# Performance work log

Measured on AMD Instinct MI355X. Metric: run time of the kernel, lower is better.

Reference implementation:

```python
import jax, jax.numpy as jnp
import numpy as np

IN_FEATURES = 8192
OUT_FEATURES = 8192
BITS = 4
TILE = 16
M_TOKENS = 64  # small token count -> dequant-traffic dominated (memory regime)
SCALE_BLOCK = 128


def setup_inputs() -> dict:
    key = jax.random.key(0)
    k1, k2, k3, k4, k5, k6 = jax.random.split(key, 6)
    tiles_k = IN_FEATURES // TILE
    tiles_n = OUT_FEATURES // TILE
    packed_bytes = 256 * BITS // 8  # 128 bytes per 16x16 tile for 4-bit
    x = jax.random.normal(k1, (M_TOKENS, IN_FEATURES), dtype=jnp.float32)
    packed_indices = jax.random.randint(k2, (tiles_k, tiles_n, packed_bytes), 0, 256, dtype=jnp.int32)
    scales = jax.random.uniform(k3, ((IN_FEATURES + SCALE_BLOCK - 1) // SCALE_BLOCK, OUT_FEATURES), dtype=jnp.float32, minval=0.5, maxval=1.5)
    su = jax.random.normal(k4, (IN_FEATURES,), dtype=jnp.float32)
    sv = jax.random.normal(k5, (OUT_FEATURES,), dtype=jnp.float32)
    grid = jax.random.normal(k6, (2 ** BITS,), dtype=jnp.float32)  # trellis codebook grid
    return {"x": x, "packed_indices": packed_indices, "scales": scales, "su": su, "sv": sv, "grid": grid}


def _dequantize(packed_indices, scales, su, sv, grid):
    # packed_indices: [tiles_k, tiles_n, packed_bytes] byte values (0..255)
    tk, tn, pb = packed_indices.shape
    bits = (pb * 8) // (TILE * TILE)
    # unpack bytes -> bits (little-endian within byte), then group into bits-per-index
    bitplane = (packed_indices[..., None] >> jnp.arange(8, dtype=jnp.int32)) & 1  # [tk, tn, pb, 8]
    idx = (bitplane.reshape(tk, tn, TILE * TILE, bits)
           * (2 ** jnp.arange(bits, dtype=jnp.int32))).sum(-1)  # [tk, tn, 256]
    vals = grid[idx].reshape(tk, tn, TILE, TILE)  # tile element order: (k_in_tile, n_in_tile)
    # assemble full weight laid out [K_in, N_out]
    W = vals.transpose(0, 2, 1, 3).reshape(tk * TILE, tn * TILE)
    # per-128-row-block scales over the K dim
    nb = scales.shape[0]
    W = (W.reshape(nb, SCALE_BLOCK, tn * TILE) * scales[:, None, :]).reshape(tk * TILE, tn * TILE)
    # per-row (su) and per-column (sv) scale/sign vectors
    W = W * su[:, None] * sv[None, :]
    return W  # [in_features, out_features]


def reference(x, packed_indices, scales, su, sv, grid):
    W = _dequantize(packed_indices, scales, su, sv, grid)  # [K, N]
    # torch: x.view(-1, K) @ weights[N, K].T  ==  x @ W[K, N]
    lead = x.shape[:-1]
    out = x.reshape(-1, W.shape[0]) @ W
    return out.reshape(*lead, W.shape[1])
```

## Files before the change

kernel.cpp:

```cpp
#include <hip/hip_runtime.h>

typedef float f32x4 __attribute__((ext_vector_type(4)));
typedef __bf16 bf16x8 __attribute__((ext_vector_type(8)));

#define K_FEAT 8192
#define N_FEAT 8192
#define M_TOK 64
#define TILES_N 512
#define TILES_K 512
#define WROWSTRIDE 40
#define LG_KSPLIT 3
#define KSPLIT 8
#define NSTEP 32

__device__ __forceinline__ unsigned short f2bf(float f) {
    unsigned int u = __builtin_bit_cast(unsigned int, f);
    u = (u + 0x7FFFu + ((u >> 16) & 1u)) >> 16;
    return (unsigned short)u;
}
__device__ __forceinline__ float bf2f(unsigned short h) {
    return __builtin_bit_cast(float, (unsigned int)h << 16);
}

__global__ void __launch_bounds__(256)
prep_x_kernel(const float* __restrict__ x, const float* __restrict__ su,
              unsigned short* __restrict__ xb)
{
    int i = blockIdx.x * 256 + threadIdx.x;
    const float4* x4 = (const float4*)x;
    const float4* su4 = (const float4*)su;
    float4 xv = x4[i];
    float4 s4 = su4[i & (K_FEAT / 4 - 1)];
    ushort4 o;
    o.x = f2bf(xv.x * s4.x);
    o.y = f2bf(xv.y * s4.y);
    o.z = f2bf(xv.z * s4.z);
    o.w = f2bf(xv.w * s4.w);
    ((ushort4*)xb)[i] = o;
}

__global__ void __launch_bounds__(256)
trellis_main(const int* __restrict__ packed,
             const float* __restrict__ scales,
             const float* __restrict__ sv,
             const float* __restrict__ grid,
             const unsigned short* __restrict__ xb,
             unsigned short* __restrict__ partials)
{
    __shared__ unsigned int table[256];
    __shared__ unsigned short wlds[2][64 * WROWSTRIDE];
    __shared__ float slds[8 * 64];

    const int tid = threadIdx.x;
    const int bid = blockIdx.x;
    const int s = bid & (KSPLIT - 1);
    const int ng = bid >> LG_KSPLIT;
    const int col0 = ng * 64;
    const int nt0 = ng * 4;
    const int ktile0 = s * (TILES_K / KSPLIT);

    const int tau = tid >> 5;
    const int dkt = tau >> 2;
    const int dnt_s = tau & 3;
    const int w = tid & 31;
    const int c = w & 7;
    const int g = w >> 3;

    const int* pb = packed
        + ((size_t)(ktile0 + dkt) * TILES_N + (nt0 + dnt_s)) * 128 + c + 32 * g;
    const int stepstride = 2 * TILES_N * 128;

    const int wave = tid >> 6;
    const int lane = tid & 63;
    const int ln15 = lane & 15;
    const int kgrp = (lane >> 4) * 8;
    const unsigned short* xrow = xb + (size_t)(wave * 16 + ln15) * K_FEAT;

    {
        float lo = grid[tid & 15];
        float hi = grid[(tid >> 4) & 15];
        table[tid] = (unsigned int)f2bf(lo) | ((unsigned int)f2bf(hi) << 16);
    }
    {
        const int kb0 = s * 8;
        slds[tid]       = scales[(size_t)(kb0 + (tid >> 6)) * N_FEAT + col0 + (tid & 63)];
        slds[tid + 256] = scales[(size_t)(kb0 + 4 + (tid >> 6)) * N_FEAT + col0 + (tid & 63)];
    }

    int ld0 = pb[0], ld1 = pb[8], ld2 = pb[16], ld3 = pb[24];
    uint4 ra = *(const uint4*)(xrow + ktile0 * 16 + kgrp);

    f32x4 acc[4], acc2[4];
    for (int d = 0; d < 4; ++d)
        for (int j = 0; j < 4; ++j) { acc[d][j] = 0.f; acc2[d][j] = 0.f; }

    __syncthreads();

    for (int t = 0; t < NSTEP; ++t) {
        int n0 = 0, n1 = 0, n2 = 0, n3 = 0;
        if (t + 1 < NSTEP) {
            const int* pn = pb + (size_t)(t + 1) * stepstride;
            n0 = pn[0]; n1 = pn[8]; n2 = pn[16]; n3 = pn[24];
        }

        unsigned int t0 = table[ld0 & 255];
        unsigned int t1 = table[ld1 & 255];
        unsigned int t2 = table[ld2 & 255];
        unsigned int t3 = table[ld3 & 255];
        unsigned int w0 = (t0 & 0xFFFFu) | (t1 << 16);
        unsigned int w1 = (t2 & 0xFFFFu) | (t3 << 16);
        unsigned int w2 = (t0 >> 16)     | (t1 & 0xFFFF0000u);
        unsigned int w3 = (t2 >> 16)     | (t3 & 0xFFFF0000u);
        {
            int nrow = dnt_s * 16 + 2 * c;
            int koff = dkt * 16 + 4 * g;
            unsigned short* dst = &wlds[t & 1][nrow * WROWSTRIDE + koff];
            *(uint2*)dst = make_uint2(w0, w1);
            *(uint2*)(dst + WROWSTRIDE) = make_uint2(w2, w3);
        }

        __builtin_amdgcn_sched_barrier(0);
        asm volatile("s_waitcnt lgkmcnt(0)" ::: "memory");
        __builtin_amdgcn_s_barrier();
        __builtin_amdgcn_sched_barrier(0);

        int k0n = ktile0 * 16 + (t + 1 < NSTEP ? (t + 1) : 0) * 32;
        uint4 ran = *(const uint4*)(xrow + k0n + kgrp);

        bf16x8 a = __builtin_bit_cast(bf16x8, ra);
        const unsigned short* wbase = &wlds[t & 1][0];
        for (int d = 0; d < 4; ++d) {
            bf16x8 b = *(const bf16x8*)(wbase + (d * 16 + ln15) * WROWSTRIDE + kgrp);
            acc2[d] = __builtin_amdgcn_mfma_f32_16x16x32_bf16(a, b, acc2[d], 0, 0, 0);
        }
        ra = ran;
        ld0 = n0; ld1 = n1; ld2 = n2; ld3 = n3;

        if ((t & 3) == 3) {
            const float* srow = slds + (t >> 2) * 64 + ln15;
            for (int d = 0; d < 4; ++d) {
                float sc = srow[d * 16];
                acc[d] += acc2[d] * sc;
                for (int j = 0; j < 4; ++j) acc2[d][j] = 0.f;
            }
        }
    }

    unsigned short* pout = partials + (size_t)s * (M_TOK * N_FEAT);
    const int rbase = (lane >> 4) * 4;
    for (int d = 0; d < 4; ++d) {
        int n = col0 + d * 16 + ln15;
        float svv = sv[n];
        for (int j = 0; j < 4; ++j) {
            int m = wave * 16 + rbase + j;
            pout[(size_t)m * N_FEAT + n] = f2bf(acc[d][j] * svv);
        }
    }
}

__global__ void __launch_bounds__(256)
reduce_kernel(const unsigned short* __restrict__ partials, float* __restrict__ out)
{
    int i = blockIdx.x * 256 + threadIdx.x;
    const uint4* p = (const uint4*)partials;
    float acc[8];
    for (int e = 0; e < 8; ++e) acc[e] = 0.f;
    for (int k = 0; k < KSPLIT; ++k) {
        uint4 v = p[(size_t)k * (M_TOK * N_FEAT / 8) + i];
        unsigned int uu[4] = {v.x, v.y, v.z, v.w};
        for (int q = 0; q < 4; ++q) {
            acc[2 * q]     += bf2f((unsigned short)(uu[q] & 0xFFFFu));
            acc[2 * q + 1] += bf2f((unsigned short)(uu[q] >> 16));
        }
    }
    float4 o0 = make_float4(acc[0], acc[1], acc[2], acc[3]);
    float4 o1 = make_float4(acc[4], acc[5], acc[6], acc[7]);
    ((float4*)out)[2 * i]     = o0;
    ((float4*)out)[2 * i + 1] = o1;
}

extern "C" void kernel_launch(void* const* d_in, const int* in_sizes, int n_in,
                              void* d_out, int out_size, void* d_ws, size_t ws_size,
                              hipStream_t stream)
{
    const float* x      = (const float*)d_in[0];
    const int*   packed = (const int*)d_in[1];
    const float* scales = (const float*)d_in[2];
    const float* su     = (const float*)d_in[3];
    const float* sv     = (const float*)d_in[4];
    const float* grid   = (const float*)d_in[5];
    float* out = (float*)d_out;

    unsigned short* xb = (unsigned short*)d_ws;
    const size_t xb_bytes = (size_t)M_TOK * K_FEAT * 2;
    unsigned short* partials = (unsigned short*)((char*)d_ws + xb_bytes);

    prep_x_kernel<<<(M_TOK * K_FEAT / 4) / 256, 256, 0, stream>>>(x, su, xb);
    trellis_main<<<(N_FEAT / 64) * KSPLIT, 256, 0, stream>>>(
        packed, scales, sv, grid, xb, partials);
    reduce_kernel<<<(M_TOK * N_FEAT / 8) / 256, 256, 0, stream>>>(partials, out);
}
```

Baseline: 38.04 us.

## Fuse split-K reduction into main kernel via last-block atomic counter; deepen packed prefetch

Removes the separate reduce kernel. Each block increments a per-column-group counter, and the last of the KSPLIT blocks sums the bf16 partials and writes the fp32 output. This saves a launch and its tail, at the cost of an added memset, fences and a serialized reduction tail inside the last block. The packed-index prefetch is also deepened to two steps ahead so more load latency is hidden, at the cost of more registers.

```diff
diff --git a/kernel.cpp b/kernel.cpp
--- a/kernel.cpp
+++ b/kernel.cpp
@@ -12,6 +12,7 @@
 #define LG_KSPLIT 3
 #define KSPLIT 8
 #define NSTEP 32
+#define NGROUPS (N_FEAT / 64)
 
 __device__ __forceinline__ unsigned short f2bf(float f) {
     unsigned int u = __builtin_bit_cast(unsigned int, f);
@@ -45,11 +46,14 @@
              const float* __restrict__ sv,
              const float* __restrict__ grid,
              const unsigned short* __restrict__ xb,
-             unsigned short* __restrict__ partials)
+             unsigned short* __restrict__ partials,
+             int* __restrict__ counters,
+             float* __restrict__ out)
 {
     __shared__ unsigned int table[256];
     __shared__ unsigned short wlds[2][64 * WROWSTRIDE];
     __shared__ float slds[8 * 64];
+    __shared__ int is_last;
 
     const int tid = threadIdx.x;
     const int bid = blockIdx.x;
@@ -87,7 +91,9 @@
         slds[tid + 256] = scales[(size_t)(kb0 + 4 + (tid >> 6)) * N_FEAT + col0 + (tid & 63)];
     }
 
-    int ld0 = pb[0], ld1 = pb[8], ld2 = pb[16], ld3 = pb[24];
+    int a0 = pb[0], a1 = pb[8], a2 = pb[16], a3 = pb[24];
+    const int* p1 = pb + stepstride;
+    int b0 = p1[0], b1 = p1[8], b2 = p1[16], b3 = p1[24];
     uint4 ra = *(const uint4*)(xrow + ktile0 * 16 + kgrp);
 
     f32x4 acc[4], acc2[4];
@@ -97,16 +103,14 @@
     __syncthreads();
 
     for (int t = 0; t < NSTEP; ++t) {
-        int n0 = 0, n1 = 0, n2 = 0, n3 = 0;
-        if (t + 1 < NSTEP) {
-            const int* pn = pb + (size_t)(t + 1) * stepstride;
-            n0 = pn[0]; n1 = pn[8]; n2 = pn[16]; n3 = pn[24];
-        }
-
-        unsigned int t0 = table[ld0 & 255];
-        unsigned int t1 = table[ld1 & 255];
-        unsigned int t2 = table[ld2 & 255];
-        unsigned int t3 = table[ld3 & 255];
+        const int tc = (t + 2 < NSTEP) ? (t + 2) : (NSTEP - 1);
+        const int* pn = pb + (size_t)tc * stepstride;
+        int c0 = pn[0], c1 = pn[8], c2 = pn[16], c3 = pn[24];
+
+        unsigned int t0 = table[a0 & 255];
+        unsigned int t1 = table[a1 & 255];
+        unsigned int t2 = table[a2 & 255];
+        unsigned int t3 = table[a3 & 255];
         unsigned int w0 = (t0 & 0xFFFFu) | (t1 << 16);
         unsigned int w1 = (t2 & 0xFFFFu) | (t3 << 16);
         unsigned int w2 = (t0 >> 16)     | (t1 & 0xFFFF0000u);
@@ -134,7 +138,8 @@
             acc2[d] = __builtin_amdgcn_mfma_f32_16x16x32_bf16(a, b, acc2[d], 0, 0, 0);
         }
         ra = ran;
-        ld0 = n0; ld1 = n1; ld2 = n2; ld3 = n3;
+        a0 = b0; a1 = b1; a2 = b2; a3 = b3;
+        b0 = c0; b1 = c1; b2 = c2; b3 = c3;
 
         if ((t & 3) == 3) {
             const float* srow = slds + (t >> 2) * 64 + ln15;
@@ -156,27 +161,34 @@
             pout[(size_t)m * N_FEAT + n] = f2bf(acc[d][j] * svv);
         }
     }
-}
-
-__global__ void __launch_bounds__(256)
-reduce_kernel(const unsigned short* __restrict__ partials, float* __restrict__ out)
-{
-    int i = blockIdx.x * 256 + threadIdx.x;
-    const uint4* p = (const uint4*)partials;
-    float acc[8];
-    for (int e = 0; e < 8; ++e) acc[e] = 0.f;
-    for (int k = 0; k < KSPLIT; ++k) {
-        uint4 v = p[(size_t)k * (M_TOK * N_FEAT / 8) + i];
-        unsigned int uu[4] = {v.x, v.y, v.z, v.w};
-        for (int q = 0; q < 4; ++q) {
-            acc[2 * q]     += bf2f((unsigned short)(uu[q] & 0xFFFFu));
-            acc[2 * q + 1] += bf2f((unsigned short)(uu[q] >> 16));
-        }
-    }
-    float4 o0 = make_float4(acc[0], acc[1], acc[2], acc[3]);
-    float4 o1 = make_float4(acc[4], acc[5], acc[6], acc[7]);
-    ((float4*)out)[2 * i]     = o0;
-    ((float4*)out)[2 * i + 1] = o1;
+
+    __syncthreads();
+    if (tid == 0) {
+        __threadfence();
+        is_last = (atomicAdd(&counters[ng], 1) == KSPLIT - 1);
+    }
+    __syncthreads();
+    if (is_last) {
+        __threadfence();
+        const int c8 = tid & 7;
+        for (int it = 0; it < 2; ++it) {
+            int m = (tid >> 3) + 32 * it;
+            float acc8[8];
+            for (int e = 0; e < 8; ++e) acc8[e] = 0.f;
+            for (int s2 = 0; s2 < KSPLIT; ++s2) {
+                uint4 v = *(const uint4*)(partials
+                    + ((size_t)s2 * M_TOK + m) * N_FEAT + col0 + c8 * 8);
+                unsigned int uu[4] = {v.x, v.y, v.z, v.w};
+                for (int q = 0; q < 4; ++q) {
+                    acc8[2 * q]     += bf2f((unsigned short)(uu[q] & 0xFFFFu));
+                    acc8[2 * q + 1] += bf2f((unsigned short)(uu[q] >> 16));
+                }
+            }
+            float* op = out + (size_t)m * N_FEAT + col0 + c8 * 8;
+            ((float4*)op)[0] = make_float4(acc8[0], acc8[1], acc8[2], acc8[3]);
+            ((float4*)op)[1] = make_float4(acc8[4], acc8[5], acc8[6], acc8[7]);
+        }
+    }
 }
 
 extern "C" void kernel_launch(void* const* d_in, const int* in_sizes, int n_in,
@@ -194,9 +206,11 @@
     unsigned short* xb = (unsigned short*)d_ws;
     const size_t xb_bytes = (size_t)M_TOK * K_FEAT * 2;
     unsigned short* partials = (unsigned short*)((char*)d_ws + xb_bytes);
-
+    const size_t part_bytes = (size_t)KSPLIT * M_TOK * N_FEAT * 2;
+    int* counters = (int*)((char*)d_ws + xb_bytes + part_bytes);
+
+    hipMemsetAsync(counters, 0, NGROUPS * sizeof(int), stream);
     prep_x_kernel<<<(M_TOK * K_FEAT / 4) / 256, 256, 0, stream>>>(x, su, xb);
-    trellis_main<<<(N_FEAT / 64) * KSPLIT, 256, 0, stream>>>(
-        packed, scales, sv, grid, xb, partials);
-    reduce_kernel<<<(M_TOK * N_FEAT / 8) / 256, 256, 0, stream>>>(partials, out);
-}
+    trellis_main<<<NGROUPS * KSPLIT, 256, 0, stream>>>(
+        packed, scales, sv, grid, xb, partials, counters, out);
+}
```

New measurement: 114.0 us. 200% more time.

## Software-pipeline dequant to LDS one step ahead with triple buffering

Applied to the files above, without the earlier changes.

Restructures the main loop so the weight tile for step t+1 is dequantized and written to LDS while the MFMAs for step t use B fragments already held in registers. A third LDS buffer is added and the packed-index prefetch distance is extended to two steps, so the barrier now sits after the MFMAs instead of in front of them. The goal is to hide LDS write, barrier and read latency behind matrix work. In exchange it uses more LDS and registers, and the prologue and epilogue logic become more complex.

```diff
diff --git a/kernel.cpp b/kernel.cpp
--- a/kernel.cpp
+++ b/kernel.cpp
@@ -48,7 +48,7 @@
              unsigned short* __restrict__ partials)
 {
     __shared__ unsigned int table[256];
-    __shared__ unsigned short wlds[2][64 * WROWSTRIDE];
+    __shared__ unsigned short wlds[3][64 * WROWSTRIDE];
     __shared__ float slds[8 * 64];
 
     const int tid = threadIdx.x;
@@ -70,6 +70,10 @@
         + ((size_t)(ktile0 + dkt) * TILES_N + (nt0 + dnt_s)) * 128 + c + 32 * g;
     const int stepstride = 2 * TILES_N * 128;
 
+    const int nrow = dnt_s * 16 + 2 * c;
+    const int koff = dkt * 16 + 4 * g;
+    const int wof = nrow * WROWSTRIDE + koff;
+
     const int wave = tid >> 6;
     const int lane = tid & 63;
     const int ln15 = lane & 15;
@@ -96,13 +100,7 @@
 
     __syncthreads();
 
-    for (int t = 0; t < NSTEP; ++t) {
-        int n0 = 0, n1 = 0, n2 = 0, n3 = 0;
-        if (t + 1 < NSTEP) {
-            const int* pn = pb + (size_t)(t + 1) * stepstride;
-            n0 = pn[0]; n1 = pn[8]; n2 = pn[16]; n3 = pn[24];
-        }
-
+    {
         unsigned int t0 = table[ld0 & 255];
         unsigned int t1 = table[ld1 & 255];
         unsigned int t2 = table[ld2 & 255];
@@ -111,30 +109,57 @@
         unsigned int w1 = (t2 & 0xFFFFu) | (t3 << 16);
         unsigned int w2 = (t0 >> 16)     | (t1 & 0xFFFF0000u);
         unsigned int w3 = (t2 >> 16)     | (t3 & 0xFFFF0000u);
-        {
-            int nrow = dnt_s * 16 + 2 * c;
-            int koff = dkt * 16 + 4 * g;
-            unsigned short* dst = &wlds[t & 1][nrow * WROWSTRIDE + koff];
+        unsigned short* dst = &wlds[0][wof];
+        *(uint2*)dst = make_uint2(w0, w1);
+        *(uint2*)(dst + WROWSTRIDE) = make_uint2(w2, w3);
+    }
+    {
+        const int* p1 = pb + stepstride;
+        ld0 = p1[0]; ld1 = p1[8]; ld2 = p1[16]; ld3 = p1[24];
+    }
+
+    __builtin_amdgcn_sched_barrier(0);
+    asm volatile("s_waitcnt lgkmcnt(0)" ::: "memory");
+    __builtin_amdgcn_s_barrier();
+    __builtin_amdgcn_sched_barrier(0);
+
+    bf16x8 fb0, fb1, fb2, fb3;
+    {
+        const unsigned short* rb = &wlds[0][0];
+        fb0 = *(const bf16x8*)(rb + (0 * 16 + ln15) * WROWSTRIDE + kgrp);
+        fb1 = *(const bf16x8*)(rb + (1 * 16 + ln15) * WROWSTRIDE + kgrp);
+        fb2 = *(const bf16x8*)(rb + (2 * 16 + ln15) * WROWSTRIDE + kgrp);
+        fb3 = *(const bf16x8*)(rb + (3 * 16 + ln15) * WROWSTRIDE + kgrp);
+    }
+
+    for (int t = 0; t < NSTEP; ++t) {
+        const int tc = (t + 2 < NSTEP) ? (t + 2) : (NSTEP - 1);
+        const int* pn = pb + (size_t)tc * stepstride;
+        int n0 = pn[0], n1 = pn[8], n2 = pn[16], n3 = pn[24];
+        const int t1i = (t + 1 < NSTEP) ? (t + 1) : (NSTEP - 1);
+        uint4 ran = *(const uint4*)(xrow + ktile0 * 16 + t1i * 32 + kgrp);
+
+        unsigned short* wb = &wlds[(t + 1) % 3][0];
+
+        if (t + 1 < NSTEP) {
+            unsigned int t0 = table[ld0 & 255];
+            unsigned int t1 = table[ld1 & 255];
+            unsigned int t2 = table[ld2 & 255];
+            unsigned int t3 = table[ld3 & 255];
+            unsigned int w0 = (t0 & 0xFFFFu) | (t1 << 16);
+            unsigned int w1 = (t2 & 0xFFFFu) | (t3 << 16);
+            unsigned int w2 = (t0 >> 16)     | (t1 & 0xFFFF0000u);
+            unsigned int w3 = (t2 >> 16)     | (t3 & 0xFFFF0000u);
+            unsigned short* dst = wb + wof;
             *(uint2*)dst = make_uint2(w0, w1);
             *(uint2*)(dst + WROWSTRIDE) = make_uint2(w2, w3);
         }
 
-        __builtin_amdgcn_sched_barrier(0);
-        asm volatile("s_waitcnt lgkmcnt(0)" ::: "memory");
-        __builtin_amdgcn_s_barrier();
-        __builtin_amdgcn_sched_barrier(0);
-
-        int k0n = ktile0 * 16 + (t + 1 < NSTEP ? (t + 1) : 0) * 32;
-        uint4 ran = *(const uint4*)(xrow + k0n + kgrp);
-
-        bf16x8 a = __builtin_bit_cast(bf16x8, ra);
-        const unsigned short* wbase = &wlds[t & 1][0];
-        for (int d = 0; d < 4; ++d) {
-            bf16x8 b = *(const bf16x8*)(wbase + (d * 16 + ln15) * WROWSTRIDE + kgrp);
-            acc2[d] = __builtin_amdgcn_mfma_f32_16x16x32_bf16(a, b, acc2[d], 0, 0, 0);
-        }
-        ra = ran;
-        ld0 = n0; ld1 = n1; ld2 = n2; ld3 = n3;
+        bf16x8 aa = __builtin_bit_cast(bf16x8, ra);
+        acc2[0] = __builtin_amdgcn_mfma_f32_16x16x32_bf16(aa, fb0, acc2[0], 0, 0, 0);
+        acc2[1] = __builtin_amdgcn_mfma_f32_16x16x32_bf16(aa, fb1, acc2[1], 0, 0, 0);
+        acc2[2] = __builtin_amdgcn_mfma_f32_16x16x32_bf16(aa, fb2, acc2[2], 0, 0, 0);
+        acc2[3] = __builtin_amdgcn_mfma_f32_16x16x32_bf16(aa, fb3, acc2[3], 0, 0, 0);
 
         if ((t & 3) == 3) {
             const float* srow = slds + (t >> 2) * 64 + ln15;
@@ -144,6 +169,21 @@
                 for (int j = 0; j < 4; ++j) acc2[d][j] = 0.f;
             }
         }
+
+        if (t + 1 < NSTEP) {
+            __builtin_amdgcn_sched_barrier(0);
+            asm volatile("s_waitcnt lgkmcnt(0)" ::: "memory");
+            __builtin_amdgcn_s_barrier();
+            __builtin_amdgcn_sched_barrier(0);
+
+            fb0 = *(const bf16x8*)(wb + (0 * 16 + ln15) * WROWSTRIDE + kgrp);
+            fb1 = *(const bf16x8*)(wb + (1 * 16 + ln15) * WROWSTRIDE + kgrp);
+            fb2 = *(const bf16x8*)(wb + (2 * 16 + ln15) * WROWSTRIDE + kgrp);
+            fb3 = *(const bf16x8*)(wb + (3 * 16 + ln15) * WROWSTRIDE + kgrp);
+        }
+
+        ra = ran;
+        ld0 = n0; ld1 = n1; ld2 = n2; ld3 = n3;
     }
 
     unsigned short* pout = partials + (size_t)s * (M_TOK * N_FEAT);
```

New measurement: 38.66 us. About the same (+1.6%).
